# Optimization experiments

Measured on AMD Instinct MI355X. Metric: run time of the kernel, lower is better.

Reference implementation:

```python
import jax, jax.numpy as jnp
import numpy as np

DIM = 1024
QKV_DIM = 64      # per-head dim
NUM_HEADS = 16
NUM_TOKENS = 1024
BATCH = 8
SCALE = QKV_DIM ** (-0.5)


def setup_inputs() -> dict:
    key = jax.random.key(0)
    k1, k2, k3 = jax.random.split(key, 3)
    x = jax.random.normal(k1, (BATCH, NUM_TOKENS, DIM), dtype=jnp.float32)
    # qkv Linear (no bias): dim -> 3 * num_heads * qkv_dim
    W_qkv = jax.random.normal(k2, (DIM, 3 * NUM_HEADS * QKV_DIM), dtype=jnp.float32) * (DIM ** -0.5)
    # reg parameter initialized to ones / num_tokens (as in nn.Parameter init)
    reg = jnp.ones((1, NUM_HEADS, NUM_TOKENS, NUM_TOKENS), dtype=jnp.float32) / NUM_TOKENS
    W_proj = jax.random.normal(k3, (NUM_HEADS * QKV_DIM, DIM), dtype=jnp.float32) * ((NUM_HEADS * QKV_DIM) ** -0.5)
    b_proj = jnp.zeros((DIM,), dtype=jnp.float32)
    return {"x": x, "W_qkv": W_qkv, "reg": reg, "W_proj": W_proj, "b_proj": b_proj}


def reference(x, W_qkv, reg, W_proj, b_proj) -> jnp.ndarray:
    B, N, C = x.shape
    H, D = NUM_HEADS, QKV_DIM
    qkv = (x @ W_qkv).reshape(B, N, 3, H, D)          # [B,N,3,H,D]
    qkv = jnp.transpose(qkv, (2, 0, 3, 1, 4))         # [3,B,H,N,D]
    q, k, v = qkv[0], qkv[1], qkv[2]
    attn = jnp.einsum('bhnd,bhmd->bhnm', q, k) * SCALE  # [B,H,N,N]
    attn = jax.nn.softmax(attn, axis=-1)
    attn = attn + reg                                   # post-softmax learned bias (broadcast over batch)
    # dropout p=0.0 -> identity
    out = jnp.einsum('bhnm,bhmd->bhnd', attn, v)        # [B,H,N,D]
    out = jnp.transpose(out, (0, 2, 1, 3)).reshape(B, N, H * D)
    return out @ W_proj + b_proj
```

## Files before the change

kernel.cpp:

```cpp
#include <hip/hip_runtime.h>
#include <hip/hip_bf16.h>

typedef __attribute__((ext_vector_type(8))) short short8;
typedef __attribute__((ext_vector_type(4))) float floatx4;

#define ATTN_C1 (0.125f * 1.44269504088896f)

__device__ inline unsigned short f2bf(float f){
  __hip_bfloat16 h = __float2bfloat16(f);
  return *reinterpret_cast<unsigned short*>(&h);
}
__device__ inline float bf2f(unsigned short u){
  __hip_bfloat16 h;
  *reinterpret_cast<unsigned short*>(&h) = u;
  return __bfloat162float(h);
}

__device__ inline bool inputs_are_bf16(const unsigned short* reg_u16){
  return reg_u16[0] == (unsigned short)0x3A80;
}

__device__ inline void gl_lds16(const void* g, void* lds_base){
  __builtin_amdgcn_global_load_lds(
      (const __attribute__((address_space(1))) void*)(unsigned long long)(uintptr_t)g,
      (__attribute__((address_space(3))) void*)(unsigned int)(uintptr_t)lds_base,
      16, 0, 0);
}

__global__ __launch_bounds__(256) void cvt_x(const void* __restrict__ in,
                                             unsigned short* __restrict__ out,
                                             const unsigned short* __restrict__ flagsrc){
  const bool isb = inputs_are_bf16(flagsrc);
  int i = (blockIdx.x*256 + threadIdx.x) * 8;
  if (isb){
    *(short8*)(out + i) = *(const short8*)((const unsigned short*)in + i);
  } else {
    const floatx4* p = (const floatx4*)((const float*)in + i);
    floatx4 f0 = p[0], f1 = p[1];
    short8 s;
    s[0]=(short)f2bf(f0[0]); s[1]=(short)f2bf(f0[1]); s[2]=(short)f2bf(f0[2]); s[3]=(short)f2bf(f0[3]);
    s[4]=(short)f2bf(f1[0]); s[5]=(short)f2bf(f1[1]); s[6]=(short)f2bf(f1[2]); s[7]=(short)f2bf(f1[3]);
    *(short8*)(out + i) = s;
  }
}

__global__ void transpose_any(const void* __restrict__ in,
                              unsigned short* __restrict__ out, int R, int C,
                              const unsigned short* __restrict__ flagsrc){
  const bool isb = inputs_are_bf16(flagsrc);
  __shared__ unsigned short t[32][33];
  int bx = blockIdx.x*32, by = blockIdx.y*32;
  int tx = threadIdx.x, ty = threadIdx.y;
  const unsigned short* in16 = (const unsigned short*)in;
  const float* inf = (const float*)in;
  #pragma unroll
  for (int i=0;i<32;i+=8){
    size_t idx = (size_t)(by+ty+i)*C + bx+tx;
    t[ty+i][tx] = isb ? in16[idx] : f2bf(inf[idx]);
  }
  __syncthreads();
  #pragma unroll
  for (int i=0;i<32;i+=8) out[(size_t)(bx+ty+i)*R + by+tx] = t[tx][ty+i];
}

__global__ __launch_bounds__(512, 2) void gemm_qkv(
    const unsigned short* __restrict__ A,
    const unsigned short* __restrict__ Bt,
    unsigned short* __restrict__ Qo,
    unsigned short* __restrict__ Ko,
    unsigned short* __restrict__ Vt)
{
  __shared__ __align__(16) unsigned short L[4][2][16][512];
  const int m0 = blockIdx.x*256, n0 = blockIdx.y*256;
  const int tid = threadIdx.x, lane = tid & 63, wave = tid >> 6;
  const int lm = lane & 15, lg = lane >> 4;
  const int wr = wave >> 2, wc = wave & 3;

  const int ib0 = wave*2, ib1 = wave*2+1;
  const unsigned short* gA0 = A  + (size_t)(m0 + ib0*16 + lm)*1024 + lg*8;
  const unsigned short* gA1 = A  + (size_t)(m0 + ib1*16 + lm)*1024 + lg*8;
  const unsigned short* gB0 = Bt + (size_t)(n0 + ib0*16 + lm)*1024 + lg*8;
  const unsigned short* gB1 = Bt + (size_t)(n0 + ib1*16 + lm)*1024 + lg*8;

#define QKV_STAGE(u_) do{                                   \
    int s_ = (u_) & 3;                                      \
    gl_lds16(gA0 + (u_)*32, &L[s_][0][ib0][0]);             \
    gl_lds16(gA1 + (u_)*32, &L[s_][0][ib1][0]);             \
    gl_lds16(gB0 + (u_)*32, &L[s_][1][ib0][0]);             \
    gl_lds16(gB1 + (u_)*32, &L[s_][1][ib1][0]);             \
  }while(0)

  floatx4 acc[8][4] = {};

#define QKV_BODY(u_) do{                                                     \
    const unsigned short* As_ = &L[(u_)&3][0][0][0];                         \
    const unsigned short* Bs_ = &L[(u_)&3][1][0][0];                         \
    short8 av[8], bv[4];                                                     \
    _Pragma("unroll")                                                        \
    for (int i=0;i<8;i++) av[i] = *(const short8*)(As_ + (wr*8+i)*512 + lane*8); \
    _Pragma("unroll")                                                        \
    for (int j=0;j<4;j++) bv[j] = *(const short8*)(Bs_ + (wc*4+j)*512 + lane*8); \
    __builtin_amdgcn_s_setprio(1);                                           \
    _Pragma("unroll")                                                        \
    for (int i=0;i<8;i++)                                                    \
      _Pragma("unroll")                                                      \
      for (int j=0;j<4;j++)                                                  \
        acc[i][j] = __builtin_amdgcn_mfma_f32_16x16x32_bf16(av[i], bv[j], acc[i][j], 0,0,0); \
    __builtin_amdgcn_s_setprio(0);                                           \
  }while(0)

  QKV_STAGE(0);
  QKV_STAGE(1);
  asm volatile("s_waitcnt vmcnt(4)" ::: "memory");
  __builtin_amdgcn_s_barrier();
  asm volatile("" ::: "memory");

  for (int u=0; u<30; ++u){
    QKV_STAGE(u+2);
    QKV_BODY(u);
    asm volatile("s_waitcnt vmcnt(4)" ::: "memory");
    __builtin_amdgcn_s_barrier();
    asm volatile("" ::: "memory");
  }
  QKV_BODY(30);
  asm volatile("s_waitcnt vmcnt(0)" ::: "memory");
  __builtin_amdgcn_s_barrier();
  asm volatile("" ::: "memory");
  QKV_BODY(31);

#undef QKV_STAGE
#undef QKV_BODY

  const int t = n0 >> 10;
  unsigned short* outp = (t==0)?Qo:((t==1)?Ko:Vt);
  const float scl = (t==0) ? ATTN_C1 : 1.0f;
  #pragma unroll
  for (int i=0;i<8;i++)
    #pragma unroll
    for (int j=0;j<4;j++)
      #pragma unroll
      for (int r=0;r<4;r++){
        int grow = m0 + wr*128 + i*16 + lg*4 + r;
        int gcol = n0 + wc*64  + j*16 + lm;
        int b = grow >> 10, n = grow & 1023;
        int h = (gcol >> 6) & 15, d = gcol & 63;
        unsigned short uv = f2bf(acc[i][j][r] * scl);
        if (t < 2) outp[((size_t)(b*16+h)*1024 + n)*64 + d] = uv;
        else       outp[((size_t)(b*16+h)*64 + d)*1024 + n] = uv;
      }
}

__global__ __launch_bounds__(256) void rv_gemm(
    const void* __restrict__ Reg,
    const unsigned short* __restrict__ Vt,
    const unsigned short* __restrict__ flagsrc,
    unsigned short* __restrict__ RV)
{
  const bool isb = inputs_are_bf16(flagsrc);
  __shared__ __align__(16) unsigned short As[128][72];
  __shared__ __align__(16) unsigned short Bs[128][72];
  const int h = blockIdx.z;
  const int m0 = blockIdx.x*128, c0 = blockIdx.y*128;
  const int tid = threadIdx.x, lane = tid & 63, wave = tid >> 6;
  const int wm = (wave>>1)*64, wn = (wave&1)*64;
  const int lm = lane & 15, lg = lane >> 4;

  const size_t regoff = (size_t)h*1024*1024;

  floatx4 acc[4][4] = {};
  for (int k0=0; k0<1024; k0+=64){
    #pragma unroll
    for (int i=0;i<4;i++){
      int c = tid + 256*i;
      int row = c >> 3;
      int off = (c & 7) << 3;
      if (isb){
        *reinterpret_cast<short8*>(&As[row][off]) =
          *reinterpret_cast<const short8*>((const unsigned short*)Reg + regoff + (size_t)(m0+row)*1024 + k0 + off);
      } else {
        const float* Rf = (const float*)Reg + regoff;
        const floatx4* p = (const floatx4*)(Rf + (size_t)(m0+row)*1024 + k0 + off);
        floatx4 f0 = p[0], f1 = p[1];
        short8 s;
        s[0]=(short)f2bf(f0[0]); s[1]=(short)f2bf(f0[1]); s[2]=(short)f2bf(f0[2]); s[3]=(short)f2bf(f0[3]);
        s[4]=(short)f2bf(f1[0]); s[5]=(short)f2bf(f1[1]); s[6]=(short)f2bf(f1[2]); s[7]=(short)f2bf(f1[3]);
        *reinterpret_cast<short8*>(&As[row][off]) = s;
      }
      int bd = c0 + row;
      const unsigned short* vrow = Vt + ((size_t)((bd>>6)*16 + h)*64 + (bd&63))*1024;
      *reinterpret_cast<short8*>(&Bs[row][off]) =
        *reinterpret_cast<const short8*>(vrow + k0 + off);
    }
    __syncthreads();
    #pragma unroll
    for (int ks=0; ks<2; ks++){
      short8 av[4], bv[4];
      int ko = ks*32 + lg*8;
      #pragma unroll
      for (int i=0;i<4;i++) av[i] = *reinterpret_cast<const short8*>(&As[wm+i*16+lm][ko]);
      #pragma unroll
      for (int j=0;j<4;j++) bv[j] = *reinterpret_cast<const short8*>(&Bs[wn+j*16+lm][ko]);
      #pragma unroll
      for (int i=0;i<4;i++)
        #pragma unroll
        for (int j=0;j<4;j++)
          acc[i][j] = __builtin_amdgcn_mfma_f32_16x16x32_bf16(av[i], bv[j], acc[i][j], 0,0,0);
    }
    __syncthreads();
  }
  #pragma unroll
  for (int i=0;i<4;i++)
    #pragma unroll
    for (int j=0;j<4;j++)
      #pragma unroll
      for (int r=0;r<4;r++){
        int n   = m0 + wm + i*16 + lg*4 + r;
        int bd  = c0 + wn + j*16 + lm;
        int b = bd >> 6, d = bd & 63;
        RV[((size_t)(b*16+h)*1024 + n)*64 + d] = f2bf(acc[i][j][r]);
      }
}

__global__ __launch_bounds__(256, 4) void attn_kernel(
    const unsigned short* __restrict__ Q,
    const unsigned short* __restrict__ K,
    const unsigned short* __restrict__ Vt,
    const unsigned short* __restrict__ RV,
    unsigned short* __restrict__ A3)
{
  const int bid = blockIdx.x;
  const int w = (bid & 7)*256 + (bid >> 3);
  const int qt = w & 15, bh = w >> 4;
  const int b = bh >> 4, h = bh & 15;
  const int tid = threadIdx.x, lane = tid & 63, wave = tid >> 6;
  const int lm = lane & 15, lg = lane >> 4;
  const int q0 = qt*64 + wave*16;

  __shared__ __align__(16) unsigned char smem[32768];
  unsigned short* Kf = (unsigned short*)smem;
  unsigned short* Vf = (unsigned short*)(smem + 16384);
  unsigned char*  Pw = smem + wave*4096;

  const unsigned short* Qp = Q  + ((size_t)bh*1024 + q0)*64;
  const unsigned short* Kp = K  + (size_t)bh*1024*64;
  const unsigned short* Vp = Vt + (size_t)bh*64*1024;

  short8 a0 = *reinterpret_cast<const short8*>(Qp + lm*64 + lg*8);
  short8 a1 = *reinterpret_cast<const short8*>(Qp + lm*64 + 32 + lg*8);

  const unsigned short* kb[4]; const unsigned short* vb[4];
  unsigned short* kl[4]; unsigned short* vl[4];
  #pragma unroll
  for (int i=0;i<4;i++){
    int c = wave*4+i;
    kb[i] = Kp + (size_t)((c>>1)*16 + lm)*64 + (c&1)*32 + lg*8;
    vb[i] = Vp + (size_t)((c>>2)*16 + lm)*1024 + (c&3)*32 + lg*8;
    kl[i] = Kf + c*512;
    vl[i] = Vf + c*512;
  }

  float ps[4] = {0.f,0.f,0.f,0.f};
  floatx4 o[4] = {};

  for (int ch=0; ch<8; ch++){
    #pragma unroll
    for (int i=0;i<4;i++){
      gl_lds16(kb[i] + ch*8192, kl[i]);
      gl_lds16(vb[i] + ch*128,  vl[i]);
    }
    asm volatile("s_waitcnt vmcnt(0)" ::: "memory");
    __builtin_amdgcn_s_barrier();
    asm volatile("" ::: "memory");

    floatx4 sc[8];
    #pragma unroll
    for (int ct=0; ct<8; ct++){
      short8 b0 = *(const short8*)(Kf + (ct*2+0)*512 + lane*8);
      short8 b1 = *(const short8*)(Kf + (ct*2+1)*512 + lane*8);
      floatx4 c = {0.f,0.f,0.f,0.f};
      c = __builtin_amdgcn_mfma_f32_16x16x32_bf16(a0, b0, c, 0,0,0);
      c = __builtin_amdgcn_mfma_f32_16x16x32_bf16(a1, b1, c, 0,0,0);
      sc[ct] = c;
    }

    #pragma unroll
    for (int r=0;r<4;r++)
      #pragma unroll
      for (int ct=0;ct<8;ct++){
        float e = __builtin_amdgcn_exp2f(sc[ct][r]);
        sc[ct][r] = e;
        ps[r] += e;
      }

    __syncthreads();

    #pragma unroll
    for (int r=0;r<4;r++){
      int row = lg*4 + r;
      unsigned int rb = (unsigned)row*256;
      unsigned int xv = (unsigned)(row & 7) << 4;
      #pragma unroll
      for (int ct=0;ct<8;ct++){
        unsigned int cb = ((unsigned)(ct*32) + (unsigned)(lm*2)) ^ xv;
        *(unsigned short*)(Pw + rb + cb) = f2bf(sc[ct][r]);
      }
    }
    #pragma unroll
    for (int kk=0;kk<4;kk++){
      unsigned int cb = ((unsigned)(kk*64 + lg*16)) ^ ((unsigned)(lm & 7) << 4);
      short8 a = *(const short8*)(Pw + (unsigned)lm*256 + cb);
      #pragma unroll
      for (int dt=0;dt<4;dt++){
        short8 bv = *(const short8*)(Vf + (dt*4+kk)*512 + lane*8);
        o[dt] = __builtin_amdgcn_mfma_f32_16x16x32_bf16(a, bv, o[dt], 0,0,0);
      }
    }
    __syncthreads();
  }

  #pragma unroll
  for (int r=0;r<4;r++){
    float s = ps[r];
    s += __shfl_xor(s, 1);
    s += __shfl_xor(s, 2);
    s += __shfl_xor(s, 4);
    s += __shfl_xor(s, 8);
    ps[r] = s;
  }

  const unsigned short* RVp = RV + ((size_t)bh*1024 + q0)*64;
  #pragma unroll
  for (int r=0;r<4;r++){
    int row = lg*4 + r;
    float inv = 1.0f / ps[r];
    #pragma unroll
    for (int dt=0;dt<4;dt++){
      int d = dt*16 + lm;
      float v = o[dt][r]*inv + bf2f(RVp[(size_t)row*64 + d]);
      A3[((size_t)b*1024 + q0 + row)*1024 + h*64 + d] = f2bf(v);
    }
  }
}

__global__ __launch_bounds__(256) void gemm_proj(
    const unsigned short* __restrict__ A,
    const unsigned short* __restrict__ Bt,
    const void* __restrict__ bias,
    const unsigned short* __restrict__ flagsrc,
    float* __restrict__ Out)
{
  const bool isb = inputs_are_bf16(flagsrc);
  __shared__ __align__(16) unsigned short As[8192];
  __shared__ __align__(16) unsigned short Bs[8192];
  const int m0 = blockIdx.x*128, n0 = blockIdx.y*128;
  const int tid = threadIdx.x, lane = tid & 63, wave = tid >> 6;
  const int lm = lane & 15, lg = lane >> 4;
  const int wm = (wave>>1)*64, wn = (wave&1)*64;

  floatx4 acc[4][4] = {};
  for (int k0=0; k0<1024; k0+=64){
    #pragma unroll
    for (int c=0;c<4;c++){
      int ib = wave*2 + (c>>1), ks = c & 1;
      int koff = k0 + ks*32 + lg*8;
      gl_lds16(A  + (size_t)(m0+ib*16+lm)*1024 + koff, &As[(ib*2+ks)*512]);
      gl_lds16(Bt + (size_t)(n0+ib*16+lm)*1024 + koff, &Bs[(ib*2+ks)*512]);
    }
    __syncthreads();
    #pragma unroll
    for (int ks=0; ks<2; ks++){
      short8 av[4], bv[4];
      #pragma unroll
      for (int i=0;i<4;i++)
        av[i] = *(const short8*)&As[(((wm>>4)+i)*2+ks)*512 + lane*8];
      #pragma unroll
      for (int j=0;j<4;j++)
        bv[j] = *(const short8*)&Bs[(((wn>>4)+j)*2+ks)*512 + lane*8];
      #pragma unroll
      for (int i=0;i<4;i++)
        #pragma unroll
        for (int j=0;j<4;j++)
          acc[i][j] = __builtin_amdgcn_mfma_f32_16x16x32_bf16(av[i], bv[j], acc[i][j], 0,0,0);
    }
    __syncthreads();
  }
  #pragma unroll
  for (int i=0;i<4;i++)
    #pragma unroll
    for (int j=0;j<4;j++)
      #pragma unroll
      for (int r=0;r<4;r++){
        int grow = m0 + wm + i*16 + lg*4 + r;
        int gcol = n0 + wn + j*16 + lm;
        float bv_ = isb ? bf2f(((const unsigned short*)bias)[gcol])
                        : ((const float*)bias)[gcol];
        Out[(size_t)grow*1024 + gcol] = acc[i][j][r] + bv_;
      }
}

extern "C" void kernel_launch(void* const* d_in, const int* in_sizes, int n_in,
                              void* d_out, int out_size, void* d_ws, size_t ws_size,
                              hipStream_t stream)
{
  const void* x      = d_in[0];
  const void* W_qkv  = d_in[1];
  const void* Reg    = d_in[2];
  const void* W_proj = d_in[3];
  const void* b_proj = d_in[4];
  const unsigned short* flagsrc = (const unsigned short*)Reg;

  char* ws = (char*)d_ws;
  unsigned short* Wt1 = (unsigned short*)(ws);
  unsigned short* Wt2 = (unsigned short*)(ws +  6291456);
  unsigned short* K   = (unsigned short*)(ws +  8388608);
  unsigned short* Vt  = (unsigned short*)(ws + 25165824);
  unsigned short* Q   = (unsigned short*)d_out;
  unsigned short* xb  = (unsigned short*)((char*)d_out + 16777216);
  unsigned short* A3  = (unsigned short*)d_in[0];
  unsigned short* RV  = (unsigned short*)((char*)d_in[0] + 16777216);

  transpose_any<<<dim3(96,32), dim3(32,8), 0, stream>>>(W_qkv, Wt1, 1024, 3072, flagsrc);
  transpose_any<<<dim3(32,32), dim3(32,8), 0, stream>>>(W_proj, Wt2, 1024, 1024, flagsrc);
  cvt_x<<<4096, 256, 0, stream>>>(x, xb, flagsrc);
  gemm_qkv<<<dim3(32,12), 512, 0, stream>>>(xb, Wt1, Q, K, Vt);
  rv_gemm<<<dim3(8,4,16), 256, 0, stream>>>(Reg, Vt, flagsrc, RV);
  attn_kernel<<<dim3(2048), 256, 0, stream>>>(Q, K, Vt, RV, A3);
  gemm_proj<<<dim3(64,8), 256, 0, stream>>>(A3, Wt2, b_proj, flagsrc, (float*)d_out);
}
```

Before: 428.6 us.

## Restructure QKV GEMM into phased pipeline and multi-stage pipeline projection GEMM

The QKV GEMM switches from a 4-stage ring with one barrier per K-slice to a double-buffered 64-wide K tile split into four phases. Each phase issues half of the next tile's loads between LDS reads and MFMAs, with barriers placed around the compute to interleave memory and math. The projection GEMM is rewritten from a single-buffered loop with two syncthreads per step into the same 4-stage global_load_lds pipeline the QKV GEMM used before, so loads overlap compute. This adds more barriers in QKV and more LDS in the projection kernel, which may affect occupancy.

Measured after the change: 429.5 us. No clear change (+0.2%).

```diff
diff --git a/kernel.cpp b/kernel.cpp
--- a/kernel.cpp
+++ b/kernel.cpp
@@ -70,11 +70,12 @@
     unsigned short* __restrict__ Ko,
     unsigned short* __restrict__ Vt)
 {
-  __shared__ __align__(16) unsigned short L[4][2][16][512];
+  __shared__ __align__(16) unsigned short L[2][2][16][2][512];
   const int m0 = blockIdx.x*256, n0 = blockIdx.y*256;
   const int tid = threadIdx.x, lane = tid & 63, wave = tid >> 6;
   const int lm = lane & 15, lg = lane >> 4;
   const int wr = wave >> 2, wc = wave & 3;
+  const int wr8 = wr*8, wc4 = wc*4, lane8 = lane*8;
 
   const int ib0 = wave*2, ib1 = wave*2+1;
   const unsigned short* gA0 = A  + (size_t)(m0 + ib0*16 + lm)*1024 + lg*8;
@@ -82,54 +83,68 @@
   const unsigned short* gB0 = Bt + (size_t)(n0 + ib0*16 + lm)*1024 + lg*8;
   const unsigned short* gB1 = Bt + (size_t)(n0 + ib1*16 + lm)*1024 + lg*8;
 
-#define QKV_STAGE(u_) do{                                   \
-    int s_ = (u_) & 3;                                      \
-    gl_lds16(gA0 + (u_)*32, &L[s_][0][ib0][0]);             \
-    gl_lds16(gA1 + (u_)*32, &L[s_][0][ib1][0]);             \
-    gl_lds16(gB0 + (u_)*32, &L[s_][1][ib0][0]);             \
-    gl_lds16(gB1 + (u_)*32, &L[s_][1][ib1][0]);             \
+#define QKV_STG_A(t_, ks_) do{                                          \
+    unsigned short (*Ld_)[16][2][512] = L[(t_)&1];                      \
+    gl_lds16(gA0 + (t_)*64 + (ks_)*32, &Ld_[0][ib0][ks_][0]);           \
+    gl_lds16(gA1 + (t_)*64 + (ks_)*32, &Ld_[0][ib1][ks_][0]);           \
   }while(0)
+#define QKV_STG_B(t_, ks_) do{                                          \
+    unsigned short (*Ld_)[16][2][512] = L[(t_)&1];                      \
+    gl_lds16(gB0 + (t_)*64 + (ks_)*32, &Ld_[1][ib0][ks_][0]);           \
+    gl_lds16(gB1 + (t_)*64 + (ks_)*32, &Ld_[1][ib1][ks_][0]);           \
+  }while(0)
+#define QKV_VW4 asm volatile("s_waitcnt vmcnt(4)" ::: "memory")
+#define QKV_VW0 asm volatile("s_waitcnt vmcnt(0)" ::: "memory")
+#define QKV_NOP ((void)0)
 
   floatx4 acc[8][4] = {};
-
-#define QKV_BODY(u_) do{                                                     \
-    const unsigned short* As_ = &L[(u_)&3][0][0][0];                         \
-    const unsigned short* Bs_ = &L[(u_)&3][1][0][0];                         \
-    short8 av[8], bv[4];                                                     \
-    _Pragma("unroll")                                                        \
-    for (int i=0;i<8;i++) av[i] = *(const short8*)(As_ + (wr*8+i)*512 + lane*8); \
-    _Pragma("unroll")                                                        \
-    for (int j=0;j<4;j++) bv[j] = *(const short8*)(Bs_ + (wc*4+j)*512 + lane*8); \
-    __builtin_amdgcn_s_setprio(1);                                           \
-    _Pragma("unroll")                                                        \
-    for (int i=0;i<8;i++)                                                    \
-      _Pragma("unroll")                                                      \
-      for (int j=0;j<4;j++)                                                  \
-        acc[i][j] = __builtin_amdgcn_mfma_f32_16x16x32_bf16(av[i], bv[j], acc[i][j], 0,0,0); \
-    __builtin_amdgcn_s_setprio(0);                                           \
+  short8 bv[4];
+
+#define QKV_PHASE(t_, ks_, ih_, STAGE_STMT, WAIT_STMT) do{                    \
+    const unsigned short (*Ls_)[16][2][512] = L[(t_)&1];                      \
+    short8 av[4];                                                             \
+    _Pragma("unroll")                                                         \
+    for (int i=0;i<4;i++)                                                     \
+      av[i] = *(const short8*)&Ls_[0][wr8+(ih_)*4+i][ks_][lane8];             \
+    if ((ih_) == 0){                                                          \
+      _Pragma("unroll")                                                       \
+      for (int j=0;j<4;j++)                                                   \
+        bv[j] = *(const short8*)&Ls_[1][wc4+j][ks_][lane8];                   \
+    }                                                                         \
+    STAGE_STMT;                                                               \
+    __builtin_amdgcn_s_barrier();                                             \
+    __builtin_amdgcn_s_setprio(1);                                            \
+    _Pragma("unroll")                                                         \
+    for (int i=0;i<4;i++){                                                    \
+      _Pragma("unroll")                                                       \
+      for (int j=0;j<4;j++)                                                   \
+        acc[(ih_)*4+i][j] = __builtin_amdgcn_mfma_f32_16x16x32_bf16(          \
+            av[i], bv[j], acc[(ih_)*4+i][j], 0,0,0);                          \
+    }                                                                         \
+    __builtin_amdgcn_s_setprio(0);                                            \
+    WAIT_STMT;                                                                \
+    __builtin_amdgcn_s_barrier();                                             \
   }while(0)
 
-  QKV_STAGE(0);
-  QKV_STAGE(1);
-  asm volatile("s_waitcnt vmcnt(4)" ::: "memory");
+  QKV_STG_A(0,0); QKV_STG_B(0,0);
+  QKV_STG_A(0,1); QKV_STG_B(0,1);
+  QKV_VW4;
   __builtin_amdgcn_s_barrier();
-  asm volatile("" ::: "memory");
-
-  for (int u=0; u<30; ++u){
-    QKV_STAGE(u+2);
-    QKV_BODY(u);
-    asm volatile("s_waitcnt vmcnt(4)" ::: "memory");
-    __builtin_amdgcn_s_barrier();
-    asm volatile("" ::: "memory");
-  }
-  QKV_BODY(30);
-  asm volatile("s_waitcnt vmcnt(0)" ::: "memory");
-  __builtin_amdgcn_s_barrier();
-  asm volatile("" ::: "memory");
-  QKV_BODY(31);
-
-#undef QKV_STAGE
-#undef QKV_BODY
+
+  for (int t=0; t<15; ++t){
+    QKV_PHASE(t, 0, 0, QKV_STG_A(t+1,0), QKV_NOP);
+    QKV_PHASE(t, 0, 1, QKV_STG_B(t+1,0), QKV_VW4);
+    QKV_PHASE(t, 1, 0, QKV_STG_A(t+1,1), QKV_NOP);
+    QKV_PHASE(t, 1, 1, QKV_STG_B(t+1,1), QKV_VW4);
+  }
+  QKV_PHASE(15, 0, 0, QKV_NOP, QKV_NOP);
+  QKV_PHASE(15, 0, 1, QKV_NOP, QKV_VW0);
+  QKV_PHASE(15, 1, 0, QKV_NOP, QKV_NOP);
+  QKV_PHASE(15, 1, 1, QKV_NOP, QKV_NOP);
+
+#undef QKV_PHASE
+#undef QKV_STG_A
+#undef QKV_STG_B
 
   const int t = n0 >> 10;
   unsigned short* outp = (t==0)?Qo:((t==1)?Ko:Vt);
@@ -194,17 +209,17 @@
     __syncthreads();
     #pragma unroll
     for (int ks=0; ks<2; ks++){
-      short8 av[4], bv[4];
+      short8 av[4], bvv[4];
       int ko = ks*32 + lg*8;
       #pragma unroll
       for (int i=0;i<4;i++) av[i] = *reinterpret_cast<const short8*>(&As[wm+i*16+lm][ko]);
       #pragma unroll
-      for (int j=0;j<4;j++) bv[j] = *reinterpret_cast<const short8*>(&Bs[wn+j*16+lm][ko]);
+      for (int j=0;j<4;j++) bvv[j] = *reinterpret_cast<const short8*>(&Bs[wn+j*16+lm][ko]);
       #pragma unroll
       for (int i=0;i<4;i++)
         #pragma unroll
         for (int j=0;j<4;j++)
-          acc[i][j] = __builtin_amdgcn_mfma_f32_16x16x32_bf16(av[i], bv[j], acc[i][j], 0,0,0);
+          acc[i][j] = __builtin_amdgcn_mfma_f32_16x16x32_bf16(av[i], bvv[j], acc[i][j], 0,0,0);
     }
     __syncthreads();
   }
@@ -311,8 +326,8 @@
       short8 a = *(const short8*)(Pw + (unsigned)lm*256 + cb);
       #pragma unroll
       for (int dt=0;dt<4;dt++){
-        short8 bv = *(const short8*)(Vf + (dt*4+kk)*512 + lane*8);
-        o[dt] = __builtin_amdgcn_mfma_f32_16x16x32_bf16(a, bv, o[dt], 0,0,0);
+        short8 bvv = *(const short8*)(Vf + (dt*4+kk)*512 + lane*8);
+        o[dt] = __builtin_amdgcn_mfma_f32_16x16x32_bf16(a, bvv, o[dt], 0,0,0);
       }
     }
     __syncthreads();
@@ -350,48 +365,75 @@
     float* __restrict__ Out)
 {
   const bool isb = inputs_are_bf16(flagsrc);
-  __shared__ __align__(16) unsigned short As[8192];
-  __shared__ __align__(16) unsigned short Bs[8192];
+  __shared__ __align__(16) unsigned short L[4][2][8][512];
   const int m0 = blockIdx.x*128, n0 = blockIdx.y*128;
   const int tid = threadIdx.x, lane = tid & 63, wave = tid >> 6;
   const int lm = lane & 15, lg = lane >> 4;
-  const int wm = (wave>>1)*64, wn = (wave&1)*64;
+  const int wr = wave >> 1, wc = wave & 1;
+
+  const int ib0 = wave*2, ib1 = wave*2+1;
+  const unsigned short* gA0 = A  + (size_t)(m0 + ib0*16 + lm)*1024 + lg*8;
+  const unsigned short* gA1 = A  + (size_t)(m0 + ib1*16 + lm)*1024 + lg*8;
+  const unsigned short* gB0 = Bt + (size_t)(n0 + ib0*16 + lm)*1024 + lg*8;
+  const unsigned short* gB1 = Bt + (size_t)(n0 + ib1*16 + lm)*1024 + lg*8;
+
+#define PRJ_STAGE(u_) do{                                   \
+    int s_ = (u_) & 3;                                      \
+    gl_lds16(gA0 + (u_)*32, &L[s_][0][ib0][0]);             \
+    gl_lds16(gA1 + (u_)*32, &L[s_][0][ib1][0]);             \
+    gl_lds16(gB0 + (u_)*32, &L[s_][1][ib0][0]);             \
+    gl_lds16(gB1 + (u_)*32, &L[s_][1][ib1][0]);             \
+  }while(0)
 
   floatx4 acc[4][4] = {};
-  for (int k0=0; k0<1024; k0+=64){
-    #pragma unroll
-    for (int c=0;c<4;c++){
-      int ib = wave*2 + (c>>1), ks = c & 1;
-      int koff = k0 + ks*32 + lg*8;
-      gl_lds16(A  + (size_t)(m0+ib*16+lm)*1024 + koff, &As[(ib*2+ks)*512]);
-      gl_lds16(Bt + (size_t)(n0+ib*16+lm)*1024 + koff, &Bs[(ib*2+ks)*512]);
-    }
-    __syncthreads();
-    #pragma unroll
-    for (int ks=0; ks<2; ks++){
-      short8 av[4], bv[4];
-      #pragma unroll
-      for (int i=0;i<4;i++)
-        av[i] = *(const short8*)&As[(((wm>>4)+i)*2+ks)*512 + lane*8];
-      #pragma unroll
-      for (int j=0;j<4;j++)
-        bv[j] = *(const short8*)&Bs[(((wn>>4)+j)*2+ks)*512 + lane*8];
-      #pragma unroll
-      for (int i=0;i<4;i++)
-        #pragma unroll
-        for (int j=0;j<4;j++)
-          acc[i][j] = __builtin_amdgcn_mfma_f32_16x16x32_bf16(av[i], bv[j], acc[i][j], 0,0,0);
-    }
-    __syncthreads();
-  }
+
+#define PRJ_BODY(u_) do{                                                     \
+    const unsigned short* As_ = &L[(u_)&3][0][0][0];                         \
+    const unsigned short* Bs_ = &L[(u_)&3][1][0][0];                         \
+    short8 av[4], bvv[4];                                                    \
+    _Pragma("unroll")                                                        \
+    for (int i=0;i<4;i++) av[i] = *(const short8*)(As_ + (wr*4+i)*512 + lane*8); \
+    _Pragma("unroll")                                                        \
+    for (int j=0;j<4;j++) bvv[j] = *(const short8*)(Bs_ + (wc*4+j)*512 + lane*8); \
+    __builtin_amdgcn_s_setprio(1);                                           \
+    _Pragma("unroll")                                                        \
+    for (int i=0;i<4;i++)                                                    \
+      _Pragma("unroll")                                                      \
+      for (int j=0;j<4;j++)                                                  \
+        acc[i][j] = __builtin_amdgcn_mfma_f32_16x16x32_bf16(av[i], bvv[j], acc[i][j], 0,0,0); \
+    __builtin_amdgcn_s_setprio(0);                                           \
+  }while(0)
+
+  PRJ_STAGE(0);
+  PRJ_STAGE(1);
+  asm volatile("s_waitcnt vmcnt(4)" ::: "memory");
+  __builtin_amdgcn_s_barrier();
+  asm volatile("" ::: "memory");
+
+  for (int u=0; u<30; ++u){
+    PRJ_STAGE(u+2);
+    PRJ_BODY(u);
+    asm volatile("s_waitcnt vmcnt(4)" ::: "memory");
+    __builtin_amdgcn_s_barrier();
+    asm volatile("" ::: "memory");
+  }
+  PRJ_BODY(30);
+  asm volatile("s_waitcnt vmcnt(0)" ::: "memory");
+  __builtin_amdgcn_s_barrier();
+  asm volatile("" ::: "memory");
+  PRJ_BODY(31);
+
+#undef PRJ_STAGE
+#undef PRJ_BODY
+
   #pragma unroll
   for (int i=0;i<4;i++)
     #pragma unroll
     for (int j=0;j<4;j++)
       #pragma unroll
       for (int r=0;r<4;r++){
-        int grow = m0 + wm + i*16 + lg*4 + r;
-        int gcol = n0 + wn + j*16 + lm;
+        int grow = m0 + wr*64 + i*16 + lg*4 + r;
+        int gcol = n0 + wc*64 + j*16 + lm;
         float bv_ = isb ? bf2f(((const unsigned short*)bias)[gcol])
                         : ((const float*)bias)[gcol];
         Out[(size_t)grow*1024 + gcol] = acc[i][j][r] + bv_;
```
